# Kernel optimization log

Hardware: AMD Instinct MI355X
Metric: run time of the kernel (lower is better)

Reference implementation:

```python
import jax, jax.numpy as jnp
import numpy as np

WEIGHT_BIT = 8
QMAX = 2 ** (WEIGHT_BIT - 1) - 1   # 127
QMIN = -2 ** (WEIGHT_BIT - 1)      # -128


def fake_quant_per_channel(W):
    # IBERT symmetric per-output-channel quantization of the weight matrix.
    # W: [out_features, in_features]; scale per output channel.
    max_abs = jnp.max(jnp.abs(W), axis=1, keepdims=True)
    scale = jnp.maximum(max_abs, 1e-8) / QMAX
    w_int = jnp.clip(jnp.round(W / scale), QMIN, QMAX)
    return w_int * scale


def setup_inputs() -> dict:
    key = jax.random.key(0)
    k1, k2, k3, k4 = jax.random.split(key, 4)
    B, S, D_FF, D = 16, 1024, 4096, 1024
    hidden_states = jax.random.normal(k1, (B, S, D_FF), dtype=jnp.float32)
    input_tensor = jax.random.normal(k2, (B, S, D), dtype=jnp.float32)
    W = jax.random.normal(k3, (D, D_FF), dtype=jnp.float32) * 0.02
    b = jax.random.normal(k4, (D,), dtype=jnp.float32) * 0.02
    return {"hidden_states": hidden_states, "input_tensor": input_tensor, "W": W, "b": b}


def reference(hidden_states, input_tensor, W, b):
    # QuantLinear: fake-quantized (8-bit per-channel symmetric) weight GEMM + bias.
    w_fq = fake_quant_per_channel(W)
    out = jnp.einsum("bsf,df->bsd", hidden_states, w_fq) + b  # [B, S, D]
    # dropout p=0.0 (inference) -> identity; residual add
    return out + input_tensor
```

## Files before the change

kernel.cpp:

```cpp
#include <hip/hip_runtime.h>
#include <hip/hip_bf16.h>
#include <stdint.h>


#define M_TOTAL 16384
#define KDIM    4096
#define NDIM    1024
#define BM      128
#define BN      128
#define BK      64

using f32x4  = __attribute__((ext_vector_type(4))) float;
using bf16x8 = __attribute__((ext_vector_type(8))) __bf16;
using u16x8  = __attribute__((ext_vector_type(8))) unsigned short;

__device__ __forceinline__ unsigned short f32_to_bf16_bits(float f) {
  union { float f; uint32_t u; } x; x.f = f;
  uint32_t r = x.u + 0x7FFFu + ((x.u >> 16) & 1u);
  return (unsigned short)(r >> 16);
}

__device__ __forceinline__ void async_copy16(const void* g, void* l) {
  __builtin_amdgcn_global_load_lds(
      (const __attribute__((address_space(1))) void*)g,
      (__attribute__((address_space(3))) void*)l,
      16, 0, 0);
}

__global__ __launch_bounds__(256) void quantize_w_kernel(
    const float* __restrict__ W, unsigned short* __restrict__ Bq) {
  const int row = blockIdx.x;
  const int t   = threadIdx.x;
  const f32x4* wv = (const f32x4*)(W + (size_t)row * KDIM);

  f32x4 v[4];
  float m = 0.0f;
#pragma unroll
  for (int i = 0; i < 4; ++i) {
    v[i] = wv[t * 4 + i];
#pragma unroll
    for (int j = 0; j < 4; ++j) m = fmaxf(m, fabsf(v[i][j]));
  }
#pragma unroll
  for (int off = 32; off >= 1; off >>= 1) m = fmaxf(m, __shfl_xor(m, off));
  __shared__ float smax[4];
  if ((t & 63) == 0) smax[t >> 6] = m;
  __syncthreads();
  m = fmaxf(fmaxf(smax[0], smax[1]), fmaxf(smax[2], smax[3]));

  const float scale = fmaxf(m, 1e-8f) / 127.0f;

  u16x8 o[2];
#pragma unroll
  for (int i = 0; i < 16; ++i) {
    float w = v[i >> 2][i & 3];
    float q = rintf(w / scale);
    q = fminf(127.0f, fmaxf(-128.0f, q));
    o[i >> 3][i & 7] = f32_to_bf16_bits(q * scale);
  }
  u16x8* dst = (u16x8*)(Bq + (size_t)row * KDIM + t * 16);
  dst[0] = o[0];
  dst[1] = o[1];
}

__global__ __launch_bounds__(256) void cast_hidden_kernel(
    const float* __restrict__ A, unsigned short* __restrict__ Ab, int n8) {
  const int stride = gridDim.x * blockDim.x;
  for (int i = blockIdx.x * blockDim.x + threadIdx.x; i < n8; i += stride) {
    const f32x4* src = (const f32x4*)A + (size_t)i * 2;
    f32x4 a = src[0], b = src[1];
    u16x8 o;
#pragma unroll
    for (int j = 0; j < 4; ++j) o[j]     = f32_to_bf16_bits(a[j]);
#pragma unroll
    for (int j = 0; j < 4; ++j) o[4 + j] = f32_to_bf16_bits(b[j]);
    ((u16x8*)Ab)[i] = o;
  }
}

__global__ __launch_bounds__(256) void gemm_bias_res_kernel(
    const unsigned short* __restrict__ A,
    const unsigned short* __restrict__ Bq,
    const float* __restrict__ bias,
    const float* __restrict__ res,
    float* __restrict__ out) {
  __shared__ unsigned short As[BM * BK];
  __shared__ unsigned short Bs[BN * BK];

  const int nwg = (M_TOTAL / BM) * (NDIM / BN);
  int bid = blockIdx.x;
  bid = (bid & 7) * (nwg >> 3) + (bid >> 3);
  const int nb = bid & 7;
  const int mb = bid >> 3;

  const int t    = threadIdx.x;
  const int lane = t & 63;
  const int wid  = t >> 6;
  const int wm   = wid >> 1;
  const int wn   = wid & 1;

  const int m0 = mb * BM;
  const int n0 = nb * BN;

  const int srow = lane >> 3;
  const int scol = (lane & 7) * 8;
  const unsigned short* ag = A  + (size_t)(m0 + wid * 32 + srow) * KDIM + scol;
  const unsigned short* bg = Bq + (size_t)(n0 + wid * 32 + srow) * KDIM + scol;

  f32x4 acc[4][4];
  const f32x4 zero = {0.f, 0.f, 0.f, 0.f};
#pragma unroll
  for (int i = 0; i < 4; ++i)
#pragma unroll
    for (int j = 0; j < 4; ++j) acc[i][j] = zero;

  const int fr = lane & 15;
  const int kg = lane >> 4;

  for (int k0 = 0; k0 < KDIM; k0 += BK) {
    if (k0) __syncthreads();
#pragma unroll
    for (int i = 0; i < 4; ++i) {
      async_copy16(ag + k0 + i * 8 * KDIM, &As[(wid * 32 + i * 8) * BK]);
      async_copy16(bg + k0 + i * 8 * KDIM, &Bs[(wid * 32 + i * 8) * BK]);
    }
    __syncthreads();

#pragma unroll
    for (int kk = 0; kk < 2; ++kk) {
      bf16x8 a[4], b[4];
#pragma unroll
      for (int i = 0; i < 4; ++i) {
        a[i] = *(const bf16x8*)&As[(wm * 64 + i * 16 + fr) * BK + kk * 32 + kg * 8];
        b[i] = *(const bf16x8*)&Bs[(wn * 64 + i * 16 + fr) * BK + kk * 32 + kg * 8];
      }
#pragma unroll
      for (int i = 0; i < 4; ++i)
#pragma unroll
        for (int j = 0; j < 4; ++j)
          acc[i][j] = __builtin_amdgcn_mfma_f32_16x16x32_bf16(a[i], b[j], acc[i][j], 0, 0, 0);
    }
  }

  const int col = lane & 15;
  const int rg  = (lane >> 4) * 4;
#pragma unroll
  for (int j = 0; j < 4; ++j) {
    const int d = n0 + wn * 64 + j * 16 + col;
    const float bb = bias[d];
#pragma unroll
    for (int i = 0; i < 4; ++i) {
      const int mrow = m0 + wm * 64 + i * 16 + rg;
#pragma unroll
      for (int r = 0; r < 4; ++r) {
        const size_t idx = (size_t)(mrow + r) * NDIM + d;
        out[idx] = acc[i][j][r] + bb + res[idx];
      }
    }
  }
}

extern "C" void kernel_launch(void* const* d_in, const int* in_sizes, int n_in,
                              void* d_out, int out_size, void* d_ws, size_t ws_size,
                              hipStream_t stream) {
  const float* hidden = (const float*)d_in[0];
  const float* resid  = (const float*)d_in[1];
  const float* W      = (const float*)d_in[2];
  const float* bias   = (const float*)d_in[3];
  float* out          = (float*)d_out;

  unsigned short* Abf = (unsigned short*)d_ws;
  unsigned short* Bq  = Abf + (size_t)M_TOTAL * KDIM;

  quantize_w_kernel<<<NDIM, 256, 0, stream>>>(W, Bq);
  cast_hidden_kernel<<<2048, 256, 0, stream>>>(hidden, Abf, (M_TOTAL * KDIM) / 8);
  gemm_bias_res_kernel<<<(M_TOTAL / BM) * (NDIM / BN), 256, 0, stream>>>(Abf, Bq, bias, resid, out);
}
```

Before: 663.6 us.

## Restructure GEMM into 256x256 double-buffered, swizzled, phased MFMA pipeline

Replaces the 128x128 single-buffered GEMM with a 256x256 tile kernel using 512 threads and double-buffered LDS (128KB). The next K tile is prefetched while the current one is consumed, and LDS columns are XOR-swizzled to avoid bank conflicts. The MFMA work is split into four phases with barriers and setprio to interleave memory and math. Larger tiles raise arithmetic intensity. The costs are heavy LDS use, more registers for accumulators, occupancy limited to one block per CU, and fewer workgroups (256).

```diff
diff --git a/kernel.cpp b/kernel.cpp
--- a/kernel.cpp
+++ b/kernel.cpp
@@ -6,9 +6,12 @@
 #define M_TOTAL 16384
 #define KDIM    4096
 #define NDIM    1024
-#define BM      128
-#define BN      128
+#define BM      256
+#define BN      256
 #define BK      64
+#define NT      (KDIM / BK)
+#define BUF_BYTES 65536
+#define B_OFF   32768
 
 using f32x4  = __attribute__((ext_vector_type(4))) float;
 using bf16x8 = __attribute__((ext_vector_type(8))) __bf16;
@@ -78,86 +81,128 @@
   }
 }
 
-__global__ __launch_bounds__(256) void gemm_bias_res_kernel(
+__global__ __launch_bounds__(512, 2) void gemm_8phase_kernel(
     const unsigned short* __restrict__ A,
     const unsigned short* __restrict__ Bq,
     const float* __restrict__ bias,
     const float* __restrict__ res,
     float* __restrict__ out) {
-  __shared__ unsigned short As[BM * BK];
-  __shared__ unsigned short Bs[BN * BK];
+  __shared__ char smem[2 * BUF_BYTES];
 
   const int nwg = (M_TOTAL / BM) * (NDIM / BN);
   int bid = blockIdx.x;
   bid = (bid & 7) * (nwg >> 3) + (bid >> 3);
-  const int nb = bid & 7;
-  const int mb = bid >> 3;
-
-  const int t    = threadIdx.x;
-  const int lane = t & 63;
-  const int wid  = t >> 6;
-  const int wm   = wid >> 1;
-  const int wn   = wid & 1;
-
-  const int m0 = mb * BM;
-  const int n0 = nb * BN;
-
-  const int srow = lane >> 3;
-  const int scol = (lane & 7) * 8;
-  const unsigned short* ag = A  + (size_t)(m0 + wid * 32 + srow) * KDIM + scol;
-  const unsigned short* bg = Bq + (size_t)(n0 + wid * 32 + srow) * KDIM + scol;
-
-  f32x4 acc[4][4];
-  const f32x4 zero = {0.f, 0.f, 0.f, 0.f};
-#pragma unroll
-  for (int i = 0; i < 4; ++i)
-#pragma unroll
-    for (int j = 0; j < 4; ++j) acc[i][j] = zero;
+  const int nb = bid & 3;
+  const int mb = bid >> 2;
+  const int m0 = mb * BM, n0 = nb * BN;
+
+  const int tid  = threadIdx.x;
+  const int lane = tid & 63;
+  const int wid  = tid >> 6;
+  const int wm   = wid >> 2;
+  const int wn   = wid & 3;
+
+  const int srow  = lane >> 3;
+  const int scol8 = (lane & 7) ^ (srow & 7);
+  const unsigned short* agp[4];
+  const unsigned short* bgp[4];
+#pragma unroll
+  for (int i = 0; i < 4; ++i) {
+    agp[i] = A  + (size_t)(m0 + i * 64 + wid * 8 + srow) * KDIM + scol8 * 8;
+    bgp[i] = Bq + (size_t)(n0 + i * 64 + wid * 8 + srow) * KDIM + scol8 * 8;
+  }
+
+#define STAGE(BUFBASE, K0) do {                                              \
+    _Pragma("unroll")                                                        \
+    for (int i_ = 0; i_ < 4; ++i_) {                                         \
+      async_copy16(agp[i_] + (K0), (BUFBASE) + (i_ * 64 + wid * 8) * 128);   \
+      async_copy16(bgp[i_] + (K0), (BUFBASE) + B_OFF + (i_ * 64 + wid * 8) * 128); \
+    }                                                                        \
+  } while (0)
 
   const int fr = lane & 15;
   const int kg = lane >> 4;
-
-  for (int k0 = 0; k0 < KDIM; k0 += BK) {
-    if (k0) __syncthreads();
-#pragma unroll
-    for (int i = 0; i < 4; ++i) {
-      async_copy16(ag + k0 + i * 8 * KDIM, &As[(wid * 32 + i * 8) * BK]);
-      async_copy16(bg + k0 + i * 8 * KDIM, &Bs[(wid * 32 + i * 8) * BK]);
-    }
-    __syncthreads();
-
-#pragma unroll
-    for (int kk = 0; kk < 2; ++kk) {
-      bf16x8 a[4], b[4];
-#pragma unroll
-      for (int i = 0; i < 4; ++i) {
-        a[i] = *(const bf16x8*)&As[(wm * 64 + i * 16 + fr) * BK + kk * 32 + kg * 8];
-        b[i] = *(const bf16x8*)&Bs[(wn * 64 + i * 16 + fr) * BK + kk * 32 + kg * 8];
-      }
-#pragma unroll
-      for (int i = 0; i < 4; ++i)
-#pragma unroll
-        for (int j = 0; j < 4; ++j)
-          acc[i][j] = __builtin_amdgcn_mfma_f32_16x16x32_bf16(a[i], b[j], acc[i][j], 0, 0, 0);
-    }
+  const int cs0 = ((kg)     ^ (fr & 7)) * 16;
+  const int cs1 = ((kg + 4) ^ (fr & 7)) * 16;
+  const int baseA = (wm * 128 + fr) * 128;
+  const int baseB = B_OFF + (wn * 64 + fr) * 128;
+
+  f32x4 acc[8][4];
+  const f32x4 zero = {0.f, 0.f, 0.f, 0.f};
+#pragma unroll
+  for (int i = 0; i < 8; ++i)
+#pragma unroll
+    for (int j = 0; j < 4; ++j) acc[i][j] = zero;
+
+#define LDA4(MB, CS) do {                                                    \
+    _Pragma("unroll")                                                        \
+    for (int q_ = 0; q_ < 4; ++q_)                                           \
+      a[q_] = *(const bf16x8*)(cur + baseA + ((MB) + q_) * 2048 + (CS));     \
+  } while (0)
+#define LDB4(CS) do {                                                        \
+    _Pragma("unroll")                                                        \
+    for (int q_ = 0; q_ < 4; ++q_)                                           \
+      b[q_] = *(const bf16x8*)(cur + baseB + q_ * 2048 + (CS));              \
+  } while (0)
+#define MFMA16(MB) do {                                                      \
+    __builtin_amdgcn_s_setprio(1);                                           \
+    _Pragma("unroll")                                                        \
+    for (int mi_ = 0; mi_ < 4; ++mi_)                                        \
+      _Pragma("unroll")                                                      \
+      for (int nj_ = 0; nj_ < 4; ++nj_)                                      \
+        acc[(MB) + mi_][nj_] = __builtin_amdgcn_mfma_f32_16x16x32_bf16(      \
+            a[mi_], b[nj_], acc[(MB) + mi_][nj_], 0, 0, 0);                  \
+    __builtin_amdgcn_s_setprio(0);                                           \
+  } while (0)
+
+  STAGE(smem, 0);
+  asm volatile("s_waitcnt vmcnt(0)" ::: "memory");
+  __builtin_amdgcn_s_barrier();
+
+  for (int tt = 0; tt < NT; ++tt) {
+    char* cur = smem + (tt & 1) * BUF_BYTES;
+    char* nxt = smem + ((tt + 1) & 1) * BUF_BYTES;
+    bf16x8 a[4], b[4];
+
+    if (tt + 1 < NT) STAGE(nxt, (tt + 1) * BK);
+    LDA4(0, cs0); LDB4(cs0);
+    MFMA16(0);
+    __builtin_amdgcn_s_barrier();
+
+    LDA4(4, cs0);
+    MFMA16(4);
+    __builtin_amdgcn_s_barrier();
+
+    LDA4(0, cs1); LDB4(cs1);
+    MFMA16(0);
+    __builtin_amdgcn_s_barrier();
+
+    LDA4(4, cs1);
+    MFMA16(4);
+    asm volatile("s_waitcnt vmcnt(0)" ::: "memory");
+    __builtin_amdgcn_s_barrier();
   }
 
   const int col = lane & 15;
   const int rg  = (lane >> 4) * 4;
 #pragma unroll
-  for (int j = 0; j < 4; ++j) {
-    const int d = n0 + wn * 64 + j * 16 + col;
+  for (int nj = 0; nj < 4; ++nj) {
+    const int d = n0 + wn * 64 + nj * 16 + col;
     const float bb = bias[d];
 #pragma unroll
-    for (int i = 0; i < 4; ++i) {
-      const int mrow = m0 + wm * 64 + i * 16 + rg;
+    for (int mi = 0; mi < 8; ++mi) {
+      const int mrow = m0 + wm * 128 + mi * 16 + rg;
 #pragma unroll
       for (int r = 0; r < 4; ++r) {
         const size_t idx = (size_t)(mrow + r) * NDIM + d;
-        out[idx] = acc[i][j][r] + bb + res[idx];
+        out[idx] = acc[mi][nj][r] + bb + res[idx];
       }
     }
   }
+#undef STAGE
+#undef LDA4
+#undef LDB4
+#undef MFMA16
 }
 
 extern "C" void kernel_launch(void* const* d_in, const int* in_sizes, int n_in,
@@ -174,5 +219,5 @@
 
   quantize_w_kernel<<<NDIM, 256, 0, stream>>>(W, Bq);
   cast_hidden_kernel<<<2048, 256, 0, stream>>>(hidden, Abf, (M_TOTAL * KDIM) / 8);
-  gemm_bias_res_kernel<<<(M_TOTAL / BM) * (NDIM / BN), 256, 0, stream>>>(Abf, Bq, bias, resid, out);
-}
+  gemm_8phase_kernel<<<(M_TOTAL / BM) * (NDIM / BN), 512, 0, stream>>>(Abf, Bq, bias, resid, out);
+}
```

After: 574.0 us. 1.16x faster.
